# Kernel tuning notes

Measured on AMD Instinct MI355X. Metric: run time of the kernel, lower is better.

Reference implementation:

```python
import jax, jax.numpy as jnp
import numpy as np

D_MODEL = 1024
N_HEADS = 16
HEAD_DIM = D_MODEL // N_HEADS


def setup_inputs() -> dict:
    key = jax.random.key(0)
    k1, k2, k3 = jax.random.split(key, 3)
    B, T = 2, 2048
    x = jax.random.normal(k1, (B, T, D_MODEL), dtype=jnp.float32)
    # causal lower-triangular mask; positions with mask==0 are blocked
    mask = jnp.tril(jnp.ones((T, T), dtype=jnp.int32))
    s = 1.0 / np.sqrt(D_MODEL)
    W_qkv = jax.random.normal(k2, (D_MODEL, 3 * D_MODEL), dtype=jnp.float32) * s
    W_out = jax.random.normal(k3, (D_MODEL, D_MODEL), dtype=jnp.float32) * s
    return {"x": x, "mask": mask, "W_qkv": W_qkv, "W_out": W_out}


def reference(x, mask, W_qkv, W_out):
    B, T, C = x.shape
    qkv = x @ W_qkv  # [B, T, 3C]
    q, k, v = jnp.split(qkv, 3, axis=-1)
    # [B, H, T, Dh]
    def heads(t):
        return t.reshape(B, T, N_HEADS, HEAD_DIM).transpose(0, 2, 1, 3)
    q, k, v = heads(q), heads(k), heads(v)
    scale = jnp.float32(1.0 / np.sqrt(HEAD_DIM))
    attn = jnp.einsum("bhqd,bhkd->bhqk", q, k) * scale  # [B,H,T,T]
    attn = jnp.where(mask == 0, jnp.float32(-jnp.inf), attn)
    attn = jax.nn.softmax(attn, axis=-1)
    out = jnp.einsum("bhqk,bhkd->bhqd", attn, v)  # [B,H,T,Dh]
    out = out.transpose(0, 2, 1, 3).reshape(B, T, C)
    return out @ W_out
```

## Files before the change

kernel.cpp:

```cpp
#include <hip/hip_runtime.h>
#include <hip/hip_bf16.h>

typedef __bf16 bf16;
typedef __bf16 bf16x4 __attribute__((ext_vector_type(4)));
typedef __bf16 bf16x8 __attribute__((ext_vector_type(8)));
typedef float f32x4 __attribute__((ext_vector_type(4)));
typedef float f32x16 __attribute__((ext_vector_type(16)));
typedef unsigned int uint4v __attribute__((ext_vector_type(4)));

__device__ __forceinline__ void gld_lds16(const void* g, void* l) {
  __builtin_amdgcn_global_load_lds(
      (const __attribute__((address_space(1))) void*)g,
      (__attribute__((address_space(3))) void*)l, 16, 0, 0);
}

__device__ __forceinline__ unsigned pkbf(float a, float b) {
  union { bf16 h[2]; unsigned u; } x;
  x.h[0] = (bf16)a; x.h[1] = (bf16)b;
  return x.u;
}

__device__ __forceinline__ void plswap2(unsigned& a, unsigned& b) {
  asm volatile("" : "+v"(a), "+v"(b));
  asm("v_permlane32_swap_b32 %0, %1" : "+v"(a), "+v"(b));
}

__device__ __forceinline__ float asf(unsigned u) { return __builtin_bit_cast(float, u); }

__device__ __forceinline__ float plmax(float x) {
  unsigned a = __builtin_bit_cast(unsigned, x), b = a;
  plswap2(a, b);
  return fmaxf(asf(a), asf(b));
}
__device__ __forceinline__ float plsum(float x) {
  unsigned a = __builtin_bit_cast(unsigned, x), b = a;
  plswap2(a, b);
  return asf(a) + asf(b);
}

__global__ __launch_bounds__(256) void cvt_kernel(const float* __restrict__ src,
                                                  bf16* __restrict__ dst, int n4) {
  int i = blockIdx.x * 256 + threadIdx.x;
  if (i < n4) {
    float4 v = ((const float4*)src)[i];
    bf16x4 o = { (bf16)v.x, (bf16)v.y, (bf16)v.z, (bf16)v.w };
    ((bf16x4*)dst)[i] = o;
  }
}

__global__ __launch_bounds__(256) void transpose_cvt_kernel(const float* __restrict__ src,
                                                            bf16* __restrict__ dst,
                                                            int R, int C) {
  __shared__ float tile[32][33];
  int tx = threadIdx.x & 31, ty = threadIdx.x >> 5;
  int bx = blockIdx.x * 32, by = blockIdx.y * 32;
#pragma unroll
  for (int j = 0; j < 32; j += 8)
    tile[ty + j][tx] = src[(size_t)(by + ty + j) * C + bx + tx];
  __syncthreads();
#pragma unroll
  for (int j = 0; j < 32; j += 8)
    dst[(size_t)(bx + ty + j) * R + by + tx] = (bf16)tile[tx][ty + j];
}

__global__ __launch_bounds__(256) void transpose_v_kernel(const bf16* __restrict__ src,
                                                          bf16* __restrict__ dst) {
  __shared__ bf16 tile[32][34];
  int bh = blockIdx.z;
  int t0 = blockIdx.x * 32;
  int d0 = blockIdx.y * 32;
  int tx = threadIdx.x & 31, ty = threadIdx.x >> 5;
  const bf16* s = src + (size_t)bh * 2048 * 64;
  bf16* d = dst + (size_t)bh * 64 * 2048;
#pragma unroll
  for (int j = 0; j < 32; j += 8)
    tile[ty + j][tx] = s[(size_t)(t0 + ty + j) * 64 + d0 + tx];
  __syncthreads();
#pragma unroll
  for (int j = 0; j < 32; j += 8)
    d[(size_t)(d0 + ty + j) * 2048 + t0 + tx] = tile[tx][ty + j];
}

template <int MODE>
__global__ __launch_bounds__(256) void gemm_kernel(
    const bf16* __restrict__ A, const bf16* __restrict__ BT,
    float* __restrict__ Cf, bf16* __restrict__ qb, bf16* __restrict__ kb,
    bf16* __restrict__ vb, int M, int N, int K) {
  __shared__ bf16 As[128 * 32];
  __shared__ bf16 Bs[128 * 32];
  const int t = threadIdx.x;
  const int w = t >> 6, l = t & 63;
  const int bm = blockIdx.y * 128, bn = blockIdx.x * 128;
  const int wr = (w >> 1) * 64, wc = (w & 1) * 64;
  const int lr = l & 15, lh = l >> 4;
  f32x4 acc[4][4] = {};

  const bf16* Ab = A + (size_t)bm * K;
  const bf16* Bb = BT + (size_t)bn * K;
  const int srow = t >> 2;
  const int scol = (t & 3) * 8;
  char* AsB = (char*)As;
  char* BsB = (char*)Bs;
  const int ldsw = w * 1024;

  for (int k0 = 0; k0 < K; k0 += 32) {
    __syncthreads();
    gld_lds16(Ab + (size_t)srow * K + k0 + scol, AsB + ldsw);
    gld_lds16(Ab + (size_t)(srow + 64) * K + k0 + scol, AsB + 4096 + ldsw);
    gld_lds16(Bb + (size_t)srow * K + k0 + scol, BsB + ldsw);
    gld_lds16(Bb + (size_t)(srow + 64) * K + k0 + scol, BsB + 4096 + ldsw);
    __syncthreads();
    bf16x8 af[4], bfr[4];
#pragma unroll
    for (int m = 0; m < 4; ++m)
      af[m] = *(const bf16x8*)(AsB + (wr + m * 16 + lr) * 64 + lh * 16);
#pragma unroll
    for (int n = 0; n < 4; ++n)
      bfr[n] = *(const bf16x8*)(BsB + (wc + n * 16 + lr) * 64 + lh * 16);
#pragma unroll
    for (int m = 0; m < 4; ++m)
#pragma unroll
      for (int n = 0; n < 4; ++n)
        acc[m][n] = __builtin_amdgcn_mfma_f32_16x16x32_bf16(af[m], bfr[n],
                                                            acc[m][n], 0, 0, 0);
  }

  const int r0 = bm + wr + (lh << 2);
  const int c0 = bn + wc + lr;
#pragma unroll
  for (int m = 0; m < 4; ++m) {
#pragma unroll
    for (int n = 0; n < 4; ++n) {
#pragma unroll
      for (int r = 0; r < 4; ++r) {
        float v = acc[m][n][r];
        int row = r0 + m * 16 + r;
        int col = c0 + n * 16;
        if (MODE == 2) {
          Cf[(size_t)row * N + col] = v;
        } else {
          int bb = row >> 11, tt = row & 2047;
          if (col < 1024) {
            int h = col >> 6, d = col & 63;
            qb[(((size_t)(bb * 16 + h)) * 2048 + tt) * 64 + d] = (bf16)v;
          } else if (col < 2048) {
            int c = col - 1024, h = c >> 6, d = c & 63;
            kb[(((size_t)(bb * 16 + h)) * 2048 + tt) * 64 + d] = (bf16)v;
          } else {
            int c = col - 2048, h = c >> 6, d = c & 63;
            vb[(((size_t)(bb * 16 + h)) * 2048 + tt) * 64 + d] = (bf16)v;
          }
        }
      }
    }
  }
}

__global__ __launch_bounds__(512, 2) void attn_kernel(const bf16* __restrict__ qb,
                                                      const bf16* __restrict__ kb,
                                                      const bf16* __restrict__ vt,
                                                      bf16* __restrict__ ao) {
  __shared__ bf16 plds[8][32][72];
  int wid = blockIdx.y * 8 + blockIdx.x;
  int swz = (wid & 7) * 32 + (wid >> 3);
  const int bh = swz >> 3;
  const int grp = swz & 7;
  const int w = threadIdx.x >> 6, l = threadIdx.x & 63;
  const int jj = grp * 4 + (w & 3);
  const int qc = (w >> 2) ? (63 - jj) : jj;
  const int qw = qc * 32;
  const int lastkt = qc;
  const int lq = l & 31, hi = l >> 5;
  const bf16* Qh = qb + (size_t)bh * 2048 * 64;
  const bf16* Kh = kb + (size_t)bh * 2048 * 64;
  const bf16* Vh = vt + (size_t)bh * 64 * 2048;
  const int bb = bh >> 4, h = bh & 15;
  const float sc2 = 0.125f * 1.4426950408889634f;

  unsigned ta = (unsigned)l, tb = (unsigned)l;
  plswap2(ta, tb);
  const bool flipped = (ta != (unsigned)(l & 31));

  bf16x8 qf[4];
#pragma unroll
  for (int c = 0; c < 4; ++c)
    qf[c] = *(const bf16x8*)(Qh + (size_t)(qw + lq) * 64 + c * 16 + hi * 8);

  f32x16 Ot0, Ot1;
#pragma unroll
  for (int r = 0; r < 16; ++r) { Ot0[r] = 0.f; Ot1[r] = 0.f; }
  float mrun = -1e30f, srun = 0.f;

  bf16x8 kA[4], vA[4], kB[4], vB[4];
#pragma unroll
  for (int c = 0; c < 4; ++c)
    kA[c] = *(const bf16x8*)(Kh + (size_t)lq * 64 + c * 16 + hi * 8);
#pragma unroll
  for (int df = 0; df < 2; ++df)
#pragma unroll
    for (int c = 0; c < 2; ++c)
      vA[df * 2 + c] = *(const bf16x8*)(Vh + (size_t)(df * 32 + lq) * 2048 + c * 16 + hi * 8);

  auto step = [&](bf16x8 (&KC)[4], bf16x8 (&VC)[4],
                  bf16x8 (&KN)[4], bf16x8 (&VN)[4], int kt) {
    const int nkv0 = (kt << 5) + 32;
#pragma unroll
    for (int c = 0; c < 4; ++c)
      KN[c] = *(const bf16x8*)(Kh + (size_t)(nkv0 + lq) * 64 + c * 16 + hi * 8);
#pragma unroll
    for (int df = 0; df < 2; ++df)
#pragma unroll
      for (int c = 0; c < 2; ++c)
        VN[df * 2 + c] = *(const bf16x8*)(Vh + (size_t)(df * 32 + lq) * 2048 + nkv0 + c * 16 + hi * 8);

    f32x16 S;
#pragma unroll
    for (int r = 0; r < 16; ++r) S[r] = 0.f;
#pragma unroll
    for (int c = 0; c < 4; ++c)
      S = __builtin_amdgcn_mfma_f32_32x32x16_bf16(KC[c], qf[c], S, 0, 0, 0);

    if (kt == lastkt) {
#pragma unroll
      for (int r = 0; r < 16; ++r) {
        int kvl = (r & 3) + 8 * (r >> 2) + 4 * hi;
        if (kvl > lq) S[r] = -1e30f;
      }
    }

    float mx[8];
#pragma unroll
    for (int i = 0; i < 8; ++i) mx[i] = fmaxf(S[2 * i], S[2 * i + 1]);
#pragma unroll
    for (int i = 0; i < 4; ++i) mx[i] = fmaxf(mx[i], mx[i + 4]);
    mx[0] = fmaxf(mx[0], mx[2]); mx[1] = fmaxf(mx[1], mx[3]);
    float smax = fmaxf(mx[0], mx[1]);
    float vmax = plmax(smax);

    float mn = mrun;
    if (!__all(vmax <= mrun + 64.0f)) {
      mn = fmaxf(mrun, vmax);
      float al = exp2f((mrun - mn) * sc2);
      srun *= al;
#pragma unroll
      for (int r = 0; r < 16; ++r) { Ot0[r] *= al; Ot1[r] *= al; }
      mrun = mn;
    }

    const float nb = -mn * sc2;
    float ps = 0.f;
    unsigned u_[8];
#pragma unroll
    for (int i = 0; i < 8; ++i) {
      float pa = exp2f(fmaf(S[2 * i], sc2, nb));
      float pb = exp2f(fmaf(S[2 * i + 1], sc2, nb));
      ps += pa + pb;
      u_[i] = pkbf(pa, pb);
    }
    srun += plsum(ps);

    unsigned a0 = u_[0], b0 = u_[2]; plswap2(a0, b0);
    unsigned a1 = u_[1], b1 = u_[3]; plswap2(a1, b1);
    unsigned a2 = u_[4], b2 = u_[6]; plswap2(a2, b2);
    unsigned a3 = u_[5], b3 = u_[7]; plswap2(a3, b3);
    unsigned w00 = flipped ? b0 : a0, w02 = flipped ? a0 : b0;
    unsigned w01 = flipped ? b1 : a1, w03 = flipped ? a1 : b1;
    unsigned w10 = flipped ? b2 : a2, w12 = flipped ? a2 : b2;
    unsigned w11 = flipped ? b3 : a3, w13 = flipped ? a3 : b3;
    uint4v f0 = {w00, w01, w02, w03};
    uint4v f1 = {w10, w11, w12, w13};
    bf16x8 pf0 = __builtin_bit_cast(bf16x8, f0);
    bf16x8 pf1 = __builtin_bit_cast(bf16x8, f1);

    Ot0 = __builtin_amdgcn_mfma_f32_32x32x16_bf16(VC[0], pf0, Ot0, 0, 0, 0);
    Ot0 = __builtin_amdgcn_mfma_f32_32x32x16_bf16(VC[1], pf1, Ot0, 0, 0, 0);
    Ot1 = __builtin_amdgcn_mfma_f32_32x32x16_bf16(VC[2], pf0, Ot1, 0, 0, 0);
    Ot1 = __builtin_amdgcn_mfma_f32_32x32x16_bf16(VC[3], pf1, Ot1, 0, 0, 0);
  };

  for (int kt = 0; kt <= lastkt; ++kt) {
    if ((kt & 1) == 0) step(kA, vA, kB, vB, kt);
    else               step(kB, vB, kA, vA, kt);
  }

  float inv = 1.0f / srun;
#pragma unroll
  for (int r = 0; r < 16; r += 2) {
    int d0 = (r & 3) + 8 * (r >> 2) + 4 * hi;
    *(unsigned*)&plds[w][lq][d0]      = pkbf(Ot0[r] * inv, Ot0[r + 1] * inv);
    *(unsigned*)&plds[w][lq][32 + d0] = pkbf(Ot1[r] * inv, Ot1[r + 1] * inv);
  }
  __builtin_amdgcn_s_waitcnt(0);

  const int q = l >> 1, dh = (l & 1) * 32;
  size_t orow = ((size_t)(bb * 2048 + qw + q)) * 1024 + h * 64 + dh;
#pragma unroll
  for (int c = 0; c < 4; ++c) {
    bf16x8 vv = *(const bf16x8*)&plds[w][q][dh + c * 8];
    *(bf16x8*)(ao + orow + c * 8) = vv;
  }
}

extern "C" void kernel_launch(void* const* d_in, const int* in_sizes, int n_in,
                              void* d_out, int out_size, void* d_ws, size_t ws_size,
                              hipStream_t stream) {
  const float* x = (const float*)d_in[0];
  const float* Wqkv = (const float*)d_in[2];
  const float* Wout = (const float*)d_in[3];
  float* out = (float*)d_out;

  char* ws = (char*)d_ws;
  bf16* xb  = (bf16*)(ws);
  bf16* wqT = (bf16*)(ws + (size_t)(8 << 20));
  bf16* woT = (bf16*)(ws + (size_t)(14 << 20));
  bf16* qb  = (bf16*)(ws + (size_t)(16 << 20));
  bf16* kb  = (bf16*)(ws + (size_t)(24 << 20));
  bf16* vt  = (bf16*)(ws + (size_t)(32 << 20));
  bf16* ao  = (bf16*)(ws + (size_t)(40 << 20));
  bf16* vb  = (bf16*)(ws + (size_t)(48 << 20));

  cvt_kernel<<<dim3(4096), dim3(256), 0, stream>>>(x, xb, 1048576);
  transpose_cvt_kernel<<<dim3(96, 32), dim3(256), 0, stream>>>(Wqkv, wqT, 1024, 3072);
  transpose_cvt_kernel<<<dim3(32, 32), dim3(256), 0, stream>>>(Wout, woT, 1024, 1024);
  gemm_kernel<1><<<dim3(24, 32), dim3(256), 0, stream>>>(xb, wqT, nullptr, qb, kb, vb,
                                                         4096, 3072, 1024);
  transpose_v_kernel<<<dim3(64, 2, 32), dim3(256), 0, stream>>>(vb, vt);
  attn_kernel<<<dim3(8, 32), dim3(512), 0, stream>>>(qb, kb, vt, ao);
  gemm_kernel<2><<<dim3(8, 32), dim3(256), 0, stream>>>(ao, woT, out, nullptr, nullptr,
                                                        nullptr, 4096, 1024, 1024);
}
```

Baseline: 227.4 us.

## Split each attention query tile's KV range across two wave halves and merge

The attention block grows from 512 to 1024 threads. Each query tile's causal KV range is split in half between two waves. The second-half wave writes its partial output accumulators, running max and running sum to a new LDS buffer, and the first-half wave merges them with a rescaled softmax combine before normalising and storing. The aim is to double the waves working on each block and shorten each wave's serial KV loop. The risks are the extra LDS (about 106 KB per block) and tighter register limits from launch_bounds(1024, 4), which could cause spills or lower occupancy.

```diff
diff --git a/kernel.cpp b/kernel.cpp
--- a/kernel.cpp
+++ b/kernel.cpp
@@ -156,20 +156,26 @@
   }
 }
 
-__global__ __launch_bounds__(512, 2) void attn_kernel(const bf16* __restrict__ qb,
-                                                      const bf16* __restrict__ kb,
-                                                      const bf16* __restrict__ vt,
-                                                      bf16* __restrict__ ao) {
+__global__ __launch_bounds__(1024, 4) void attn_kernel(const bf16* __restrict__ qb,
+                                                       const bf16* __restrict__ kb,
+                                                       const bf16* __restrict__ vt,
+                                                       bf16* __restrict__ ao) {
+  __shared__ float pmerge[8][64][34];
   __shared__ bf16 plds[8][32][72];
   int wid = blockIdx.y * 8 + blockIdx.x;
   int swz = (wid & 7) * 32 + (wid >> 3);
   const int bh = swz >> 3;
   const int grp = swz & 7;
   const int w = threadIdx.x >> 6, l = threadIdx.x & 63;
-  const int jj = grp * 4 + (w & 3);
-  const int qc = (w >> 2) ? (63 - jj) : jj;
+  const int p = w & 7;
+  const int half = w >> 3;
+  const int jj = grp * 4 + (p & 3);
+  const int qc = (p >> 2) ? (63 - jj) : jj;
   const int qw = qc * 32;
-  const int lastkt = qc;
+  const int ct = qc + 1;
+  const int hA = ct >> 1;
+  const int k0 = half ? hA : 0;
+  const int k1 = half ? ct : hA;
   const int lq = l & 31, hi = l >> 5;
   const bf16* Qh = qb + (size_t)bh * 2048 * 64;
   const bf16* Kh = kb + (size_t)bh * 2048 * 64;
@@ -192,14 +198,17 @@
   float mrun = -1e30f, srun = 0.f;
 
   bf16x8 kA[4], vA[4], kB[4], vB[4];
-#pragma unroll
-  for (int c = 0; c < 4; ++c)
-    kA[c] = *(const bf16x8*)(Kh + (size_t)lq * 64 + c * 16 + hi * 8);
-#pragma unroll
-  for (int df = 0; df < 2; ++df)
-#pragma unroll
-    for (int c = 0; c < 2; ++c)
-      vA[df * 2 + c] = *(const bf16x8*)(Vh + (size_t)(df * 32 + lq) * 2048 + c * 16 + hi * 8);
+  {
+    const int kv0 = k0 << 5;
+#pragma unroll
+    for (int c = 0; c < 4; ++c)
+      kA[c] = *(const bf16x8*)(Kh + (size_t)(kv0 + lq) * 64 + c * 16 + hi * 8);
+#pragma unroll
+    for (int df = 0; df < 2; ++df)
+#pragma unroll
+      for (int c = 0; c < 2; ++c)
+        vA[df * 2 + c] = *(const bf16x8*)(Vh + (size_t)(df * 32 + lq) * 2048 + kv0 + c * 16 + hi * 8);
+  }
 
   auto step = [&](bf16x8 (&KC)[4], bf16x8 (&VC)[4],
                   bf16x8 (&KN)[4], bf16x8 (&VN)[4], int kt) {
@@ -220,7 +229,7 @@
     for (int c = 0; c < 4; ++c)
       S = __builtin_amdgcn_mfma_f32_32x32x16_bf16(KC[c], qf[c], S, 0, 0, 0);
 
-    if (kt == lastkt) {
+    if (kt == qc) {
 #pragma unroll
       for (int r = 0; r < 16; ++r) {
         int kvl = (r & 3) + 8 * (r >> 2) + 4 * hi;
@@ -278,17 +287,43 @@
     Ot1 = __builtin_amdgcn_mfma_f32_32x32x16_bf16(VC[3], pf1, Ot1, 0, 0, 0);
   };
 
-  for (int kt = 0; kt <= lastkt; ++kt) {
-    if ((kt & 1) == 0) step(kA, vA, kB, vB, kt);
-    else               step(kB, vB, kA, vA, kt);
-  }
-
-  float inv = 1.0f / srun;
+  for (int i = 0; i < k1 - k0; ++i) {
+    int kt = k0 + i;
+    if ((i & 1) == 0) step(kA, vA, kB, vB, kt);
+    else              step(kB, vB, kA, vA, kt);
+  }
+
+  if (half) {
+    float* dst = &pmerge[p][l][0];
+#pragma unroll
+    for (int r = 0; r < 16; ++r) dst[r] = Ot0[r];
+#pragma unroll
+    for (int r = 0; r < 16; ++r) dst[16 + r] = Ot1[r];
+    dst[32] = mrun;
+    dst[33] = srun;
+    __syncthreads();
+    return;
+  }
+  __syncthreads();
+
+  const float* src = &pmerge[p][l][0];
+  float mB = src[32], sB = src[33];
+  float m = fmaxf(mrun, mB);
+  float eA = exp2f((mrun - m) * sc2);
+  float eB = exp2f((mB - m) * sc2);
+  float s = srun * eA + sB * eB;
+  float inv = 1.0f / s;
+  float fA = eA * inv, fB = eB * inv;
+#pragma unroll
+  for (int r = 0; r < 16; ++r) Ot0[r] = Ot0[r] * fA + src[r] * fB;
+#pragma unroll
+  for (int r = 0; r < 16; ++r) Ot1[r] = Ot1[r] * fA + src[16 + r] * fB;
+
 #pragma unroll
   for (int r = 0; r < 16; r += 2) {
     int d0 = (r & 3) + 8 * (r >> 2) + 4 * hi;
-    *(unsigned*)&plds[w][lq][d0]      = pkbf(Ot0[r] * inv, Ot0[r + 1] * inv);
-    *(unsigned*)&plds[w][lq][32 + d0] = pkbf(Ot1[r] * inv, Ot1[r + 1] * inv);
+    *(unsigned*)&plds[w][lq][d0]      = pkbf(Ot0[r], Ot0[r + 1]);
+    *(unsigned*)&plds[w][lq][32 + d0] = pkbf(Ot1[r], Ot1[r + 1]);
   }
   __builtin_amdgcn_s_waitcnt(0);
 
@@ -325,7 +360,7 @@
   gemm_kernel<1><<<dim3(24, 32), dim3(256), 0, stream>>>(xb, wqT, nullptr, qb, kb, vb,
                                                          4096, 3072, 1024);
   transpose_v_kernel<<<dim3(64, 2, 32), dim3(256), 0, stream>>>(vb, vt);
-  attn_kernel<<<dim3(8, 32), dim3(512), 0, stream>>>(qb, kb, vt, ao);
+  attn_kernel<<<dim3(8, 32), dim3(1024), 0, stream>>>(qb, kb, vt, ao);
   gemm_kernel<2><<<dim3(8, 32), dim3(256), 0, stream>>>(ao, woT, out, nullptr, nullptr,
                                                         nullptr, 4096, 1024, 1024);
 }
```

After: 605.6 us. 2.66x slower.
